# Kernel tuning notes

Hardware: AMD Instinct MI355X
Metric: run time of the kernel (lower is better)

The kernel has to match this reference:

```python
import jax, jax.numpy as jnp
import numpy as np

B, S, E, H = 4, 2048, 16, 4  # batch, seq, embed_dim (= n_wires), num_heads
D_K = E // H


def setup_inputs() -> dict:
    key = jax.random.key(0)
    k1, k2, k3, k4, k5 = jax.random.split(key, 5)
    return {
        "x": jax.random.normal(k1, (B, S, E), dtype=jnp.float32),
        "theta": jax.random.normal(k2, (E,), dtype=jnp.float32),
        "Wk": jax.random.normal(k3, (E, E), dtype=jnp.float32) / np.float32(np.sqrt(E)),
        "Wv": jax.random.normal(k4, (E, E), dtype=jnp.float32) / np.float32(np.sqrt(E)),
        "Wc": jax.random.normal(k5, (E, E), dtype=jnp.float32) / np.float32(np.sqrt(E)),
    }


def _split_heads(t):
    # [B, S, E] -> [B, H, S, D_K]
    b, s, _ = t.shape
    return t.reshape(b, s, H, D_K).transpose(0, 2, 1, 3)


def reference(x, theta, Wk, Wv, Wc):
    # Quantum head: RX(x_i) then RX(theta_i) on wire i from |0>, measure PauliZ.
    # Single-qubit RX rotations on disjoint wires factorize: <Z_i> = cos(x_i + theta_i).
    q = jnp.cos(x + theta)          # [B, S, E] (batched over all tokens at once)
    k = x @ Wk.T                    # nn.Linear(bias=False): x @ W^T
    v = x @ Wv.T

    qh, kh, vh = _split_heads(q), _split_heads(k), _split_heads(v)
    scale = np.float32(1.0 / np.sqrt(D_K))
    scores = jnp.einsum("bhqd,bhkd->bhqk", qh, kh) * scale  # [B, H, S, S]
    attn = jax.nn.softmax(scores, axis=-1)
    out = jnp.einsum("bhqk,bhkd->bhqd", attn, vh)           # [B, H, S, D_K]
    out = out.transpose(0, 2, 1, 3).reshape(x.shape)        # [B, S, E]
    return out @ Wc.T
```

## Files before the change

### kernel.cpp

```cpp
#include <hip/hip_runtime.h>
#include <math.h>

#define BB 4
#define SS 2048
#define EE 16
#define HH 4
#define DK 4
#define KS 8
#define NQ (BB*HH*SS)
#define KLEN (SS/KS)
#define QPT 2

#define QSCALE 0.7213475204444817f

typedef float v2f __attribute__((ext_vector_type(2)));

__global__ __launch_bounds__(512) void attn_fused(
    const float* __restrict__ x, const float* __restrict__ theta,
    const float* __restrict__ Wk, const float* __restrict__ Wv,
    float* __restrict__ accp, float* __restrict__ lp)
{
    __shared__ float skx[KLEN], sky[KLEN], skz[KLEN], skw[KLEN];
    __shared__ float svx[KLEN], svy[KLEN], svz[KLEN], svw[KLEN];

    int tid = threadIdx.x;
    int qc = blockIdx.x;
    int ks = blockIdx.y;
    int bh = blockIdx.z;
    int b = bh >> 2;
    int h = bh & 3;

    if (tid < KLEN) {
        const float4* xr = reinterpret_cast<const float4*>(
            x + ((size_t)b*SS + (size_t)ks*KLEN + tid) * EE);
        float4 x0 = xr[0], x1 = xr[1], x2 = xr[2], x3 = xr[3];
        float xv[EE] = {x0.x,x0.y,x0.z,x0.w, x1.x,x1.y,x1.z,x1.w,
                        x2.x,x2.y,x2.z,x2.w, x3.x,x3.y,x3.z,x3.w};
        float kd[DK], vd[DK];
        #pragma unroll
        for (int d = 0; d < DK; ++d) {
            float ak = 0.f, av = 0.f;
            #pragma unroll
            for (int e = 0; e < EE; ++e) {
                ak = fmaf(xv[e], Wk[(h*4+d)*EE + e], ak);
                av = fmaf(xv[e], Wv[(h*4+d)*EE + e], av);
            }
            kd[d] = ak; vd[d] = av;
        }
        skx[tid] = kd[0]; sky[tid] = kd[1]; skz[tid] = kd[2]; skw[tid] = kd[3];
        svx[tid] = vd[0]; svy[tid] = vd[1]; svz[tid] = vd[2]; svw[tid] = vd[3];
    }

    float th0 = theta[h*4+0], th1 = theta[h*4+1];
    float th2 = theta[h*4+2], th3 = theta[h*4+3];
    int s0 = qc*1024 + tid;
    float4 xq0 = *reinterpret_cast<const float4*>(x + ((size_t)b*SS + s0) * EE + h*4);
    float4 xq1 = *reinterpret_cast<const float4*>(x + ((size_t)b*SS + s0 + 512) * EE + h*4);
    float q0x = __cosf(xq0.x + th0) * QSCALE, q0y = __cosf(xq0.y + th1) * QSCALE;
    float q0z = __cosf(xq0.z + th2) * QSCALE, q0w = __cosf(xq0.w + th3) * QSCALE;
    float q1x = __cosf(xq1.x + th0) * QSCALE, q1y = __cosf(xq1.y + th1) * QSCALE;
    float q1z = __cosf(xq1.z + th2) * QSCALE, q1w = __cosf(xq1.w + th3) * QSCALE;
    v2f Q0x = {q0x,q0x}, Q0y = {q0y,q0y}, Q0z = {q0z,q0z}, Q0w = {q0w,q0w};
    v2f Q1x = {q1x,q1x}, Q1y = {q1y,q1y}, Q1z = {q1z,q1z}, Q1w = {q1w,q1w};

    __syncthreads();

    v2f a0x = {}, a0y = {}, a0z = {}, a0w = {};
    v2f a1x = {}, a1y = {}, a1z = {}, a1w = {};
    v2f l0 = {}, l1 = {};
    const float4* kx4 = reinterpret_cast<const float4*>(skx);
    const float4* ky4 = reinterpret_cast<const float4*>(sky);
    const float4* kz4 = reinterpret_cast<const float4*>(skz);
    const float4* kw4 = reinterpret_cast<const float4*>(skw);
    const float4* vx4 = reinterpret_cast<const float4*>(svx);
    const float4* vy4 = reinterpret_cast<const float4*>(svy);
    const float4* vz4 = reinterpret_cast<const float4*>(svz);
    const float4* vw4 = reinterpret_cast<const float4*>(svw);

    #pragma unroll 2
    for (int i = 0; i < KLEN/4; ++i) {
        float4 kx = kx4[i], ky = ky4[i], kz = kz4[i], kw = kw4[i];
        float4 vx = vx4[i], vy = vy4[i], vz = vz4[i], vw = vw4[i];
        v2f kx01 = {kx.x, kx.y}, kx23 = {kx.z, kx.w};
        v2f ky01 = {ky.x, ky.y}, ky23 = {ky.z, ky.w};
        v2f kz01 = {kz.x, kz.y}, kz23 = {kz.z, kz.w};
        v2f kw01 = {kw.x, kw.y}, kw23 = {kw.z, kw.w};
        v2f vx01 = {vx.x, vx.y}, vx23 = {vx.z, vx.w};
        v2f vy01 = {vy.x, vy.y}, vy23 = {vy.z, vy.w};
        v2f vz01 = {vz.x, vz.y}, vz23 = {vz.z, vz.w};
        v2f vw01 = {vw.x, vw.y}, vw23 = {vw.z, vw.w};

        v2f sc = __builtin_elementwise_fma(Q0x, kx01,
                 __builtin_elementwise_fma(Q0y, ky01,
                 __builtin_elementwise_fma(Q0z, kz01, Q0w * kw01)));
        v2f p; p.x = __builtin_amdgcn_exp2f(sc.x); p.y = __builtin_amdgcn_exp2f(sc.y);
        l0 += p;
        a0x = __builtin_elementwise_fma(p, vx01, a0x);
        a0y = __builtin_elementwise_fma(p, vy01, a0y);
        a0z = __builtin_elementwise_fma(p, vz01, a0z);
        a0w = __builtin_elementwise_fma(p, vw01, a0w);
        sc = __builtin_elementwise_fma(Q0x, kx23,
             __builtin_elementwise_fma(Q0y, ky23,
             __builtin_elementwise_fma(Q0z, kz23, Q0w * kw23)));
        p.x = __builtin_amdgcn_exp2f(sc.x); p.y = __builtin_amdgcn_exp2f(sc.y);
        l0 += p;
        a0x = __builtin_elementwise_fma(p, vx23, a0x);
        a0y = __builtin_elementwise_fma(p, vy23, a0y);
        a0z = __builtin_elementwise_fma(p, vz23, a0z);
        a0w = __builtin_elementwise_fma(p, vw23, a0w);
        sc = __builtin_elementwise_fma(Q1x, kx01,
             __builtin_elementwise_fma(Q1y, ky01,
             __builtin_elementwise_fma(Q1z, kz01, Q1w * kw01)));
        p.x = __builtin_amdgcn_exp2f(sc.x); p.y = __builtin_amdgcn_exp2f(sc.y);
        l1 += p;
        a1x = __builtin_elementwise_fma(p, vx01, a1x);
        a1y = __builtin_elementwise_fma(p, vy01, a1y);
        a1z = __builtin_elementwise_fma(p, vz01, a1z);
        a1w = __builtin_elementwise_fma(p, vw01, a1w);
        sc = __builtin_elementwise_fma(Q1x, kx23,
             __builtin_elementwise_fma(Q1y, ky23,
             __builtin_elementwise_fma(Q1z, kz23, Q1w * kw23)));
        p.x = __builtin_amdgcn_exp2f(sc.x); p.y = __builtin_amdgcn_exp2f(sc.y);
        l1 += p;
        a1x = __builtin_elementwise_fma(p, vx23, a1x);
        a1y = __builtin_elementwise_fma(p, vy23, a1y);
        a1z = __builtin_elementwise_fma(p, vz23, a1z);
        a1w = __builtin_elementwise_fma(p, vw23, a1w);
    }

    int gq0 = bh*SS + s0;
    *reinterpret_cast<float4*>(accp + ((size_t)ks*NQ + gq0)*4) =
        make_float4(a0x.x + a0x.y, a0y.x + a0y.y, a0z.x + a0z.y, a0w.x + a0w.y);
    lp[(size_t)ks*NQ + gq0] = l0.x + l0.y;
    *reinterpret_cast<float4*>(accp + ((size_t)ks*NQ + gq0 + 512)*4) =
        make_float4(a1x.x + a1x.y, a1y.x + a1y.y, a1z.x + a1z.y, a1w.x + a1w.y);
    lp[(size_t)ks*NQ + gq0 + 512] = l1.x + l1.y;
}

__global__ __launch_bounds__(64) void out_kernel(
    const float* __restrict__ accp, const float* __restrict__ lp,
    const float* __restrict__ Wc, float* __restrict__ out)
{
    int t = blockIdx.x * 64 + threadIdx.x;
    int b = t >> 11;
    int s = t & (SS - 1);

    float attn[EE];
    #pragma unroll
    for (int h = 0; h < HH; ++h) {
        int gq = (b*HH + h)*SS + s;
        float ax = 0.f, ay = 0.f, az = 0.f, aw = 0.f, l = 0.f;
        #pragma unroll
        for (int ks = 0; ks < KS; ++ks) {
            float4 a = *reinterpret_cast<const float4*>(accp + ((size_t)ks*NQ + gq)*4);
            ax += a.x; ay += a.y; az += a.z; aw += a.w;
            l += lp[(size_t)ks*NQ + gq];
        }
        float inv = 1.0f / l;
        attn[h*4+0] = ax*inv; attn[h*4+1] = ay*inv;
        attn[h*4+2] = az*inv; attn[h*4+3] = aw*inv;
    }

    float4* orow = reinterpret_cast<float4*>(out + (size_t)t * EE);
    #pragma unroll
    for (int e4 = 0; e4 < 4; ++e4) {
        float o[4];
        #pragma unroll
        for (int i = 0; i < 4; ++i) {
            int e = e4*4 + i;
            float acc = 0.f;
            #pragma unroll
            for (int j = 0; j < EE; ++j)
                acc = fmaf(attn[j], Wc[e*EE + j], acc);
            o[i] = acc;
        }
        orow[e4] = make_float4(o[0], o[1], o[2], o[3]);
    }
}

extern "C" void kernel_launch(void* const* d_in, const int* in_sizes, int n_in,
                              void* d_out, int out_size, void* d_ws, size_t ws_size,
                              hipStream_t stream)
{
    const float* x     = (const float*)d_in[0];
    const float* theta = (const float*)d_in[1];
    const float* Wk    = (const float*)d_in[2];
    const float* Wv    = (const float*)d_in[3];
    const float* Wc    = (const float*)d_in[4];
    float* out = (float*)d_out;

    float* ws   = (float*)d_ws;
    float* accp = ws;
    float* lp   = accp + (size_t)KS*NQ*4;

    attn_fused<<<dim3(2, KS, BB*HH), 512, 0, stream>>>(x, theta, Wk, Wv, accp, lp);
    out_kernel<<<dim3((BB*SS)/64), 64, 0, stream>>>(accp, lp, Wc, out);
}
```

Before: 84.51 us.

## Fuse output projection into attention kernel via last-block atomic counter

```diff
diff --git a/kernel.cpp b/kernel.cpp
--- a/kernel.cpp
+++ b/kernel.cpp
@@ -7,9 +7,9 @@
 #define HH 4
 #define DK 4
 #define KS 8
+#define QC 2
 #define NQ (BB*HH*SS)
 #define KLEN (SS/KS)
-#define QPT 2
 
 #define QSCALE 0.7213475204444817f
 
@@ -18,10 +18,13 @@
 __global__ __launch_bounds__(512) void attn_fused(
     const float* __restrict__ x, const float* __restrict__ theta,
     const float* __restrict__ Wk, const float* __restrict__ Wv,
-    float* __restrict__ accp, float* __restrict__ lp)
+    const float* __restrict__ Wc, float* __restrict__ out,
+    float* __restrict__ accp, float* __restrict__ lp,
+    unsigned int* __restrict__ cnt)
 {
     __shared__ float skx[KLEN], sky[KLEN], skz[KLEN], skw[KLEN];
     __shared__ float svx[KLEN], svy[KLEN], svz[KLEN], svw[KLEN];
+    __shared__ int sFinish;
 
     int tid = threadIdx.x;
     int qc = blockIdx.x;
@@ -135,46 +138,52 @@
     *reinterpret_cast<float4*>(accp + ((size_t)ks*NQ + gq0 + 512)*4) =
         make_float4(a1x.x + a1x.y, a1y.x + a1y.y, a1z.x + a1z.y, a1w.x + a1w.y);
     lp[(size_t)ks*NQ + gq0 + 512] = l1.x + l1.y;
-}
-
-__global__ __launch_bounds__(64) void out_kernel(
-    const float* __restrict__ accp, const float* __restrict__ lp,
-    const float* __restrict__ Wc, float* __restrict__ out)
-{
-    int t = blockIdx.x * 64 + threadIdx.x;
-    int b = t >> 11;
-    int s = t & (SS - 1);
-
-    float attn[EE];
+
+    __threadfence();
+    if (tid == 0) {
+        unsigned int old = atomicAdd(&cnt[b*QC + qc], 1u);
+        sFinish = (old == HH*KS - 1) ? 1 : 0;
+    }
+    __syncthreads();
+    if (!sFinish) return;
+    __threadfence();
+
     #pragma unroll
-    for (int h = 0; h < HH; ++h) {
-        int gq = (b*HH + h)*SS + s;
-        float ax = 0.f, ay = 0.f, az = 0.f, aw = 0.f, l = 0.f;
+    for (int j = 0; j < 2; ++j) {
+        int s = qc*1024 + tid + j*512;
+        int t = b*SS + s;
+
+        float attn[EE];
         #pragma unroll
-        for (int ks = 0; ks < KS; ++ks) {
-            float4 a = *reinterpret_cast<const float4*>(accp + ((size_t)ks*NQ + gq)*4);
-            ax += a.x; ay += a.y; az += a.z; aw += a.w;
-            l += lp[(size_t)ks*NQ + gq];
+        for (int hh = 0; hh < HH; ++hh) {
+            int gq = (b*HH + hh)*SS + s;
+            float ax = 0.f, ay = 0.f, az = 0.f, aw = 0.f, l = 0.f;
+            #pragma unroll
+            for (int k = 0; k < KS; ++k) {
+                float4 a = *reinterpret_cast<const float4*>(accp + ((size_t)k*NQ + gq)*4);
+                ax += a.x; ay += a.y; az += a.z; aw += a.w;
+                l += lp[(size_t)k*NQ + gq];
+            }
+            float inv = 1.0f / l;
+            attn[hh*4+0] = ax*inv; attn[hh*4+1] = ay*inv;
+            attn[hh*4+2] = az*inv; attn[hh*4+3] = aw*inv;
         }
-        float inv = 1.0f / l;
-        attn[h*4+0] = ax*inv; attn[h*4+1] = ay*inv;
-        attn[h*4+2] = az*inv; attn[h*4+3] = aw*inv;
-    }
-
-    float4* orow = reinterpret_cast<float4*>(out + (size_t)t * EE);
-    #pragma unroll
-    for (int e4 = 0; e4 < 4; ++e4) {
-        float o[4];
+
+        float4* orow = reinterpret_cast<float4*>(out + (size_t)t * EE);
         #pragma unroll
-        for (int i = 0; i < 4; ++i) {
-            int e = e4*4 + i;
-            float acc = 0.f;
+        for (int e4 = 0; e4 < 4; ++e4) {
+            float o[4];
             #pragma unroll
-            for (int j = 0; j < EE; ++j)
-                acc = fmaf(attn[j], Wc[e*EE + j], acc);
-            o[i] = acc;
+            for (int i = 0; i < 4; ++i) {
+                int e = e4*4 + i;
+                float acc = 0.f;
+                #pragma unroll
+                for (int jj = 0; jj < EE; ++jj)
+                    acc = fmaf(attn[jj], Wc[e*EE + jj], acc);
+                o[i] = acc;
+            }
+            orow[e4] = make_float4(o[0], o[1], o[2], o[3]);
         }
-        orow[e4] = make_float4(o[0], o[1], o[2], o[3]);
     }
 }
 
@@ -190,9 +199,11 @@
     float* out = (float*)d_out;
 
     float* ws   = (float*)d_ws;
-    float* accp = ws;
+    unsigned int* cnt = (unsigned int*)ws;
+    float* accp = ws + 64;
     float* lp   = accp + (size_t)KS*NQ*4;
 
-    attn_fused<<<dim3(2, KS, BB*HH), 512, 0, stream>>>(x, theta, Wk, Wv, accp, lp);
-    out_kernel<<<dim3((BB*SS)/64), 64, 0, stream>>>(accp, lp, Wc, out);
+    hipMemsetAsync(cnt, 0, QC*BB*sizeof(unsigned int), stream);
+    attn_fused<<<dim3(QC, KS, BB*HH), 512, 0, stream>>>(
+        x, theta, Wk, Wv, Wc, out, accp, lp, cnt);
 }
```

Result: slower. 141.8 us (+67.8%).
